# Kernel tuning notes

Measured on AMD Instinct MI355X. Metric: run time of the kernel, lower is better.

## Reference

```python
import jax, jax.numpy as jnp
import numpy as np

DIM = 1024
HEADS = 16
HEAD_DIM = DIM // HEADS
SEQ = 2048
BATCH = 2


def setup_inputs() -> dict:
    key = jax.random.key(0)
    ks = jax.random.split(key, 9)
    s = 1.0 / np.sqrt(DIM)
    mk = lambda k: jax.random.uniform(k, (DIM, DIM), jnp.float32, -s, s)
    mb = lambda k: jax.random.uniform(k, (DIM,), jnp.float32, -s, s)
    return {
        "x": jax.random.normal(ks[0], (BATCH, SEQ, DIM), jnp.float32),
        "wq": mk(ks[1]), "bq": mb(ks[2]),
        "wk": mk(ks[3]), "bk": mb(ks[4]),
        "wv": mk(ks[5]), "bv": mb(ks[6]),
        "wo": mk(ks[7]), "bo": mb(ks[8]),
    }


def reference(x, wq, bq, wk, bk, wv, bv, wo, bo):
    b, s, d = x.shape
    inv_sqrt_hd = 1.0 / np.sqrt(HEAD_DIM)
    # torch Linear: y = x @ W.T + b
    q = (x @ wq.T + bq).reshape(b, s, HEADS, HEAD_DIM)
    k = (x @ wk.T + bk).reshape(b, s, HEADS, HEAD_DIM)
    v = (x @ wv.T + bv).reshape(b, s, HEADS, HEAD_DIM)
    # scores [b, h, s, s]; NOTE: original forward never applies the causal mask buffer
    scores = jnp.einsum("bqhd,bkhd->bhqk", q, k) * inv_sqrt_hd
    a = jax.nn.softmax(scores, axis=-1)
    o = jnp.einsum("bhqk,bkhd->bqhd", a, v).reshape(b, s, d)
    o = o @ wo.T + bo
    return (o, a.mean(axis=1))
```

## Files before the change

kernel.cpp:

```cpp
#include <hip/hip_runtime.h>
#include <stdint.h>

#define DIMD 1024
#define HEADS 16
#define HD 64
#define SEQ 2048
#define BATCH 2
#define MTOT (BATCH*SEQ)

typedef __attribute__((ext_vector_type(4))) float f32x4;
typedef __attribute__((ext_vector_type(8))) short bf16x8;
typedef __attribute__((ext_vector_type(8))) unsigned short ushort8;
typedef __attribute__((ext_vector_type(4))) unsigned short usx4;

#define GL_LDS16(gp, lp) __builtin_amdgcn_global_load_lds( \
    (const __attribute__((address_space(1))) unsigned int*)(gp), \
    (__attribute__((address_space(3))) unsigned int*)(lp), 16, 0, 0)

__device__ __forceinline__ unsigned short f2bf(float f) {
    unsigned int u = __builtin_bit_cast(unsigned int, f);
    u = (u + 0x7FFFu + ((u >> 16) & 1u)) >> 16;
    return (unsigned short)u;
}
__device__ __forceinline__ float bf2f(unsigned short s) {
    unsigned int u = ((unsigned int)s) << 16;
    return __builtin_bit_cast(float, u);
}

__global__ __launch_bounds__(256) void cvt_f32_bf16(const float* __restrict__ in,
                                                    unsigned short* __restrict__ out, int n) {
    int i = (blockIdx.x * 256 + threadIdx.x) * 8;
    if (i >= n) return;
    f32x4 a = *(const f32x4*)(in + i);
    f32x4 b = *(const f32x4*)(in + i + 4);
    ushort8 o;
    o[0] = f2bf(a[0]); o[1] = f2bf(a[1]); o[2] = f2bf(a[2]); o[3] = f2bf(a[3]);
    o[4] = f2bf(b[0]); o[5] = f2bf(b[1]); o[6] = f2bf(b[2]); o[7] = f2bf(b[3]);
    *(ushort8*)(out + i) = o;
}

__global__ __launch_bounds__(256) void cvt_w4(const float* __restrict__ w0, const float* __restrict__ w1,
                                              const float* __restrict__ w2, const float* __restrict__ w3,
                                              unsigned short* __restrict__ dst) {
    const int sel = blockIdx.x >> 9;
    const float* src = sel == 0 ? w0 : sel == 1 ? w1 : sel == 2 ? w2 : w3;
    int i = ((blockIdx.x & 511) * 256 + threadIdx.x) * 8;
    f32x4 a = *(const f32x4*)(src + i);
    f32x4 b = *(const f32x4*)(src + i + 4);
    ushort8 o;
    o[0] = f2bf(a[0]); o[1] = f2bf(a[1]); o[2] = f2bf(a[2]); o[3] = f2bf(a[3]);
    o[4] = f2bf(b[0]); o[5] = f2bf(b[1]); o[6] = f2bf(b[2]); o[7] = f2bf(b[3]);
    *(ushort8*)(dst + (size_t)sel * 1048576 + i) = o;
}

template<bool F32OUT>
__device__ __forceinline__ void gemm_body(const unsigned short* __restrict__ X,
                                          const unsigned short* __restrict__ W,
                                          const float* __restrict__ bias,
                                          void* __restrict__ outp,
                                          int m0, int n0, int Nv, int Kv,
                                          unsigned short (*As)[128 * 64],
                                          unsigned short (*Bs)[64 * 64]) {
    const int tid = threadIdx.x, wid = tid >> 6;
    const int lane = tid & 63, lr = lane & 15, hi = lane >> 4;
    const int mq = (wid >> 1) * 64, nq = (wid & 1) * 32;
    const int NT = Kv >> 6;

    f32x4 acc[4][2];
    #pragma unroll
    for (int i = 0; i < 4; ++i)
        #pragma unroll
        for (int j = 0; j < 2; ++j) acc[i][j] = (f32x4){0.f, 0.f, 0.f, 0.f};

    #pragma unroll
    for (int it = 0; it < 4; ++it) {
        int li = it * 256 + tid, row = li >> 3, seg = li & 7;
        GL_LDS16(X + (size_t)(m0 + row) * Kv + ((seg ^ (row & 7)) << 3), &As[0][li * 8]);
    }
    #pragma unroll
    for (int it = 0; it < 2; ++it) {
        int li = it * 256 + tid, row = li >> 3, seg = li & 7;
        GL_LDS16(W + (size_t)(n0 + row) * Kv + ((seg ^ (row & 7)) << 3), &Bs[0][li * 8]);
    }
    __syncthreads();

    #pragma unroll 2
    for (int t = 0; t < NT; ++t) {
        const int cur = t & 1, nxt = cur ^ 1;
        if (t + 1 < NT) {
            const int k1 = (t + 1) << 6;
            #pragma unroll
            for (int it = 0; it < 4; ++it) {
                int li = it * 256 + tid, row = li >> 3, seg = li & 7;
                GL_LDS16(X + (size_t)(m0 + row) * Kv + k1 + ((seg ^ (row & 7)) << 3),
                         &As[nxt][li * 8]);
            }
            #pragma unroll
            for (int it = 0; it < 2; ++it) {
                int li = it * 256 + tid, row = li >> 3, seg = li & 7;
                GL_LDS16(W + (size_t)(n0 + row) * Kv + k1 + ((seg ^ (row & 7)) << 3),
                         &Bs[nxt][li * 8]);
            }
        }
        #pragma unroll
        for (int kk = 0; kk < 2; ++kk) {
            bf16x8 af[4], bfr[2];
            #pragma unroll
            for (int i = 0; i < 4; ++i) {
                int row = mq + 16 * i + lr;
                int seg = (kk * 4 + hi) ^ (row & 7);
                af[i] = *(const bf16x8*)(&As[cur][row * 64 + seg * 8]);
            }
            #pragma unroll
            for (int j = 0; j < 2; ++j) {
                int row = nq + 16 * j + lr;
                int seg = (kk * 4 + hi) ^ (row & 7);
                bfr[j] = *(const bf16x8*)(&Bs[cur][row * 64 + seg * 8]);
            }
            #pragma unroll
            for (int i = 0; i < 4; ++i)
                #pragma unroll
                for (int j = 0; j < 2; ++j)
                    acc[i][j] = __builtin_amdgcn_mfma_f32_16x16x32_bf16(af[i], bfr[j], acc[i][j], 0, 0, 0);
        }
        __syncthreads();
    }

    #pragma unroll
    for (int j = 0; j < 2; ++j) {
        const int col = n0 + nq + 16 * j + lr;
        const float bv = bias[col];
        #pragma unroll
        for (int i = 0; i < 4; ++i) {
            #pragma unroll
            for (int r = 0; r < 4; ++r) {
                const int row = m0 + mq + 16 * i + 4 * hi + r;
                float v = acc[i][j][r] + bv;
                if (F32OUT) ((float*)outp)[(size_t)row * Nv + col] = v;
                else        ((unsigned short*)outp)[(size_t)row * Nv + col] = f2bf(v);
            }
        }
    }
}

template<bool F32OUT>
__global__ __launch_bounds__(256, 2) void gemm_lds(const unsigned short* __restrict__ X,
                                                   const unsigned short* __restrict__ W,
                                                   const float* __restrict__ bias,
                                                   void* __restrict__ outp,
                                                   int Nv, int Kv) {
    __shared__ unsigned short As[2][128 * 64];
    __shared__ unsigned short Bs[2][64 * 64];
    gemm_body<F32OUT>(X, W, bias, outp, blockIdx.y * 128, blockIdx.x * 64, Nv, Kv, As, Bs);
}

__global__ __launch_bounds__(256, 2) void gemm_qkv(const unsigned short* __restrict__ X,
                                                   const unsigned short* __restrict__ Wall,
                                                   const float* __restrict__ b0,
                                                   const float* __restrict__ b1,
                                                   const float* __restrict__ b2,
                                                   unsigned short* __restrict__ o0,
                                                   unsigned short* __restrict__ o1,
                                                   unsigned short* __restrict__ o2) {
    __shared__ unsigned short As[2][128 * 64];
    __shared__ unsigned short Bs[2][64 * 64];
    const int sel = blockIdx.x >> 4;
    const int n0 = (blockIdx.x & 15) * 64;
    const unsigned short* W = Wall + (size_t)sel * 1048576;
    const float* bias = sel == 0 ? b0 : sel == 1 ? b1 : b2;
    unsigned short* out = sel == 0 ? o0 : sel == 1 ? o1 : o2;
    gemm_body<false>(X, W, bias, out, blockIdx.y * 128, n0, DIMD, DIMD, As, Bs);
}

__global__ __launch_bounds__(256) void transpose_v(const unsigned short* __restrict__ v,
                                                   unsigned short* __restrict__ vT) {
    __shared__ unsigned short tile[64][72];
    const int bh = blockIdx.y;
    const int b = bh >> 4, h = bh & 15;
    const int s0 = blockIdx.x * 64;
    const int t = threadIdx.x;
    #pragma unroll
    for (int it = 0; it < 2; ++it) {
        int li = it * 256 + t;
        int row = li >> 3, c8 = (li & 7) * 8;
        ushort8 val = *(const ushort8*)(v + (size_t)(b * SEQ + s0 + row) * DIMD + h * HD + c8);
        *(ushort8*)&tile[row][c8] = val;
    }
    __syncthreads();
    #pragma unroll
    for (int it = 0; it < 2; ++it) {
        int li = it * 256 + t;
        int d = li >> 3, s8 = (li & 7) * 8;
        ushort8 o;
        #pragma unroll
        for (int j = 0; j < 8; ++j) o[j] = tile[s8 + j][d];
        *(ushort8*)(vT + (size_t)(bh * HD + d) * SEQ + s0 + s8) = o;
    }
}

__global__ __launch_bounds__(256, 4) void score_pv_kernel(const unsigned short* __restrict__ Q,
                                                          const unsigned short* __restrict__ Kt,
                                                          const unsigned short* __restrict__ vT,
                                                          float* __restrict__ rlb,
                                                          unsigned short* __restrict__ attn, int b) {
    __shared__ unsigned short Ks[2][64 * 64];
    __shared__ unsigned short Vs[2][64 * 64];
    __shared__ unsigned short Es[32 * 68];
    __shared__ float ps[4][2][16];
    __shared__ float rls[32];
    const int tid = threadIdx.x, wid = tid >> 6, lane = tid & 63;
    const int lr = lane & 15, hi = lane >> 4;
    const int h = blockIdx.y;
    const int q0 = blockIdx.x * 32;
    const unsigned short* Kbase = Kt + (size_t)b * SEQ * DIMD + h * HD;
    const unsigned short* Vbase = vT + (size_t)(b * HEADS + h) * HD * SEQ;

    const unsigned short* qbase = Q + (size_t)(b * SEQ + q0) * DIMD + h * HD + 8 * hi;
    bf16x8 qb0[2], qb1[2];
    #pragma unroll
    for (int s = 0; s < 2; ++s) {
        const unsigned short* qp = qbase + (size_t)(16 * s + lr) * DIMD;
        qb0[s] = *(const bf16x8*)qp;
        qb1[s] = *(const bf16x8*)(qp + 32);
    }

    #pragma unroll
    for (int it = 0; it < 2; ++it) {
        int li = it * 256 + tid, row = li >> 3, seg = li & 7;
        GL_LDS16(Kbase + (size_t)row * DIMD + ((seg ^ (row & 7)) << 3), &Ks[0][li * 8]);
    }
    #pragma unroll
    for (int it = 0; it < 2; ++it) {
        int li = it * 256 + tid, row = li >> 3, seg = li & 7;
        GL_LDS16(Vbase + (size_t)row * SEQ + ((seg ^ (row & 7)) << 3), &Vs[0][li * 8]);
    }
    __syncthreads();

    float lsum[2] = {0.f, 0.f};
    f32x4 oacc[2];
    oacc[0] = (f32x4){0.f, 0.f, 0.f, 0.f};
    oacc[1] = (f32x4){0.f, 0.f, 0.f, 0.f};
    const int mq = (wid >> 1) * 16;
    const int nd = (wid & 1) * 32;

    for (int t = 0; t < 32; ++t) {
        const int cur = t & 1, nxt = cur ^ 1;
        if (t + 1 < 32) {
            const int kb1 = (t + 1) * 64;
            #pragma unroll
            for (int it = 0; it < 2; ++it) {
                int li = it * 256 + tid, row = li >> 3, seg = li & 7;
                GL_LDS16(Kbase + (size_t)(kb1 + row) * DIMD + ((seg ^ (row & 7)) << 3),
                         &Ks[nxt][li * 8]);
            }
            #pragma unroll
            for (int it = 0; it < 2; ++it) {
                int li = it * 256 + tid, row = li >> 3, seg = li & 7;
                GL_LDS16(Vbase + (size_t)row * SEQ + kb1 + ((seg ^ (row & 7)) << 3),
                         &Vs[nxt][li * 8]);
            }
        }
        const int krow = wid * 16 + lr;
        bf16x8 a0 = *(const bf16x8*)(&Ks[cur][krow * 64 + ((hi       ^ (krow & 7)) << 3)]);
        bf16x8 a1 = *(const bf16x8*)(&Ks[cur][krow * 64 + (((4 + hi) ^ (krow & 7)) << 3)]);
        #pragma unroll
        for (int s = 0; s < 2; ++s) {
            f32x4 acc = (f32x4){0.f, 0.f, 0.f, 0.f};
            acc = __builtin_amdgcn_mfma_f32_16x16x32_bf16(a0, qb0[s], acc, 0, 0, 0);
            acc = __builtin_amdgcn_mfma_f32_16x16x32_bf16(a1, qb1[s], acc, 0, 0, 0);
            float e0 = __expf(acc[0] * 0.125f);
            float e1 = __expf(acc[1] * 0.125f);
            float e2 = __expf(acc[2] * 0.125f);
            float e3 = __expf(acc[3] * 0.125f);
            lsum[s] += (e0 + e1) + (e2 + e3);
            usx4 pk;
            pk[0] = f2bf(e0); pk[1] = f2bf(e1); pk[2] = f2bf(e2); pk[3] = f2bf(e3);
            *(usx4*)(&Es[(16 * s + lr) * 68 + wid * 16 + 4 * hi]) = pk;
        }
        __syncthreads();

        #pragma unroll
        for (int kk = 0; kk < 2; ++kk) {
            bf16x8 ea = *(const bf16x8*)(&Es[(mq + lr) * 68 + kk * 32 + 8 * hi]);
            #pragma unroll
            for (int j = 0; j < 2; ++j) {
                int vrow = nd + 16 * j + lr;
                int seg = (kk * 4 + hi) ^ (vrow & 7);
                bf16x8 vb = *(const bf16x8*)(&Vs[cur][vrow * 64 + seg * 8]);
                oacc[j] = __builtin_amdgcn_mfma_f32_16x16x32_bf16(ea, vb, oacc[j], 0, 0, 0);
            }
        }
        __syncthreads();
    }

    #pragma unroll
    for (int s = 0; s < 2; ++s) {
        float l = lsum[s];
        l += __shfl_xor(l, 16);
        l += __shfl_xor(l, 32);
        if (lane < 16) ps[wid][s][lane] = l;
    }
    __syncthreads();
    if (tid < 32) {
        int s = tid >> 4, qq = tid & 15;
        float tot = ps[0][s][qq] + ps[1][s][qq] + ps[2][s][qq] + ps[3][s][qq];
        float r = 1.0f / tot;
        rlb[h * SEQ + q0 + 16 * s + qq] = r;
        rls[16 * s + qq] = r;
    }
    __syncthreads();

    #pragma unroll
    for (int r = 0; r < 4; ++r) {
        const int ql = mq + 4 * hi + r;
        const float rv = rls[ql];
        #pragma unroll
        for (int j = 0; j < 2; ++j)
            attn[(size_t)(b * SEQ + q0 + ql) * DIMD + h * HD + nd + 16 * j + lr] =
                f2bf(oacc[j][r] * rv);
    }
}

__global__ __launch_bounds__(256, 4) void mean_qk_kernel(const unsigned short* __restrict__ Q,
                                                         const unsigned short* __restrict__ Kt,
                                                         const float* __restrict__ rlb,
                                                         float* __restrict__ out1b, int b) {
    __shared__ unsigned short Ks[2][128 * 64];
    __shared__ unsigned short Qs[2][32 * 64];
    const int tid = threadIdx.x, wid = tid >> 6, lane = tid & 63;
    const int lr = lane & 15, hi = lane >> 4;
    const int k0 = blockIdx.x * 128;
    const int q0 = blockIdx.y * 32;
    const unsigned short* Kb2 = Kt + (size_t)b * SEQ * DIMD;
    const unsigned short* Qb2 = Q + (size_t)(b * SEQ + q0) * DIMD;

    f32x4 acc[2][2];
    #pragma unroll
    for (int c = 0; c < 2; ++c)
        #pragma unroll
        for (int g = 0; g < 2; ++g) acc[c][g] = (f32x4){0.f, 0.f, 0.f, 0.f};

    #pragma unroll
    for (int it = 0; it < 4; ++it) {
        int li = it * 256 + tid, row = li >> 3, seg = li & 7;
        GL_LDS16(Kb2 + (size_t)(k0 + row) * DIMD + ((seg ^ (row & 7)) << 3), &Ks[0][li * 8]);
    }
    {
        int row = tid >> 3, seg = tid & 7;
        GL_LDS16(Qb2 + (size_t)row * DIMD + ((seg ^ (row & 7)) << 3), &Qs[0][tid * 8]);
    }
    __syncthreads();

    for (int h = 0; h < HEADS; ++h) {
        const int cur = h & 1;
        if (h + 1 < HEADS) {
            const int off2 = (h + 1) * HD;
            #pragma unroll
            for (int it = 0; it < 4; ++it) {
                int li = it * 256 + tid, row = li >> 3, seg = li & 7;
                GL_LDS16(Kb2 + (size_t)(k0 + row) * DIMD + off2 + ((seg ^ (row & 7)) << 3),
                         &Ks[cur ^ 1][li * 8]);
            }
            {
                int row = tid >> 3, seg = tid & 7;
                GL_LDS16(Qb2 + (size_t)row * DIMD + off2 + ((seg ^ (row & 7)) << 3),
                         &Qs[cur ^ 1][tid * 8]);
            }
        }
        bf16x8 qb0[2], qb1[2];
        float rlv[2];
        #pragma unroll
        for (int g = 0; g < 2; ++g) {
            const int qrow = 16 * g + lr;
            qb0[g] = *(const bf16x8*)(&Qs[cur][qrow * 64 + ((hi       ^ (qrow & 7)) << 3)]);
            qb1[g] = *(const bf16x8*)(&Qs[cur][qrow * 64 + (((4 + hi) ^ (qrow & 7)) << 3)]);
            rlv[g] = rlb[h * SEQ + q0 + 16 * g + lr] * 0.0625f;
        }
        #pragma unroll
        for (int c = 0; c < 2; ++c) {
            const int krow = c * 64 + wid * 16 + lr;
            bf16x8 a0 = *(const bf16x8*)(&Ks[cur][krow * 64 + ((hi       ^ (krow & 7)) << 3)]);
            bf16x8 a1 = *(const bf16x8*)(&Ks[cur][krow * 64 + (((4 + hi) ^ (krow & 7)) << 3)]);
            #pragma unroll
            for (int g = 0; g < 2; ++g) {
                f32x4 s = (f32x4){0.f, 0.f, 0.f, 0.f};
                s = __builtin_amdgcn_mfma_f32_16x16x32_bf16(a0, qb0[g], s, 0, 0, 0);
                s = __builtin_amdgcn_mfma_f32_16x16x32_bf16(a1, qb1[g], s, 0, 0, 0);
                #pragma unroll
                for (int r = 0; r < 4; ++r)
                    acc[c][g][r] += __expf(s[r] * 0.125f) * rlv[g];
            }
        }
        __syncthreads();
    }

    #pragma unroll
    for (int c = 0; c < 2; ++c)
        #pragma unroll
        for (int g = 0; g < 2; ++g)
            *(f32x4*)(out1b + (size_t)(q0 + 16 * g + lr) * SEQ
                              + k0 + 64 * c + 16 * wid + 4 * hi) = acc[c][g];
}

extern "C" void kernel_launch(void* const* d_in, const int* in_sizes, int n_in,
                              void* d_out, int out_size, void* d_ws, size_t ws_size,
                              hipStream_t stream) {
    const float* x  = (const float*)d_in[0];
    const float* wq = (const float*)d_in[1];
    const float* bq = (const float*)d_in[2];
    const float* wk = (const float*)d_in[3];
    const float* bk = (const float*)d_in[4];
    const float* wv = (const float*)d_in[5];
    const float* bv = (const float*)d_in[6];
    const float* wo = (const float*)d_in[7];
    const float* bo = (const float*)d_in[8];

    float* o_out    = (float*)d_out;
    float* mean_out = o_out + 4194304;

    unsigned short* xb   = (unsigned short*)d_ws;
    unsigned short* wqb  = xb   + 4194304;
    unsigned short* wkb  = wqb  + 1048576;
    unsigned short* wvb  = wkb  + 1048576;
    unsigned short* wob  = wvb  + 1048576;
    unsigned short* qb   = wob  + 1048576;
    unsigned short* kb   = qb   + 4194304;
    unsigned short* vTb  = kb   + 4194304;
    unsigned short* attb = vTb  + 4194304;
    float*          rlb  = (float*)(attb + 4194304);
    unsigned short* vb   = (unsigned short*)(rlb + 65536);

    cvt_f32_bf16<<<2048, 256, 0, stream>>>(x, xb, 4194304);
    cvt_w4<<<2048, 256, 0, stream>>>(wq, wk, wv, wo, wqb);

    gemm_qkv<<<dim3(48, 32), 256, 0, stream>>>(xb, wqb, bq, bk, bv, qb, kb, vb);
    transpose_v<<<dim3(32, 32), 256, 0, stream>>>(vb, vTb);

    for (int b = 0; b < BATCH; ++b) {
        float* rl_b = rlb + b * HEADS * SEQ;
        score_pv_kernel<<<dim3(64, 16), 256, 0, stream>>>(qb, kb, vTb, rl_b, attb, b);
        mean_qk_kernel<<<dim3(16, 64), 256, 0, stream>>>(qb, kb, rl_b,
                                                         mean_out + (size_t)b * SEQ * SEQ, b);
    }

    gemm_lds<true><<<dim3(16, 32), 256, 0, stream>>>(attb, wob, bo, o_out, DIMD, DIMD);
}
```

Measured before the change: 195.2 us.

## Give each wave its own 16 queries in score_pv and merge batch launches

The attention kernel now assigns each wave a private 16-query slice of a 64-query tile. Each wave computes scores over all 64 keys, keeps its own P tile in LDS, and accumulates all 64 output dims, which removes the mid-iteration block barrier and the cross-wave row-sum reduction. The per-batch launch loop is replaced by a 3D grid so both batches run in a single launch of each kernel, which cuts launch count and tail effects. In exchange, per-thread accumulators grow and launch bounds drop to 3 blocks per CU, which lowers occupancy.

After: 202.7 us. +3.9%, slower.

```diff
diff --git a/kernel.cpp b/kernel.cpp
--- a/kernel.cpp
+++ b/kernel.cpp
@@ -198,31 +198,25 @@
     }
 }
 
-__global__ __launch_bounds__(256, 4) void score_pv_kernel(const unsigned short* __restrict__ Q,
+__global__ __launch_bounds__(256, 3) void score_pv_kernel(const unsigned short* __restrict__ Q,
                                                           const unsigned short* __restrict__ Kt,
                                                           const unsigned short* __restrict__ vT,
                                                           float* __restrict__ rlb,
-                                                          unsigned short* __restrict__ attn, int b) {
+                                                          unsigned short* __restrict__ attn) {
     __shared__ unsigned short Ks[2][64 * 64];
     __shared__ unsigned short Vs[2][64 * 64];
-    __shared__ unsigned short Es[32 * 68];
-    __shared__ float ps[4][2][16];
-    __shared__ float rls[32];
+    __shared__ unsigned short Es[4][16 * 68];
     const int tid = threadIdx.x, wid = tid >> 6, lane = tid & 63;
     const int lr = lane & 15, hi = lane >> 4;
     const int h = blockIdx.y;
-    const int q0 = blockIdx.x * 32;
+    const int b = blockIdx.z;
+    const int q0 = blockIdx.x * 64;
     const unsigned short* Kbase = Kt + (size_t)b * SEQ * DIMD + h * HD;
     const unsigned short* Vbase = vT + (size_t)(b * HEADS + h) * HD * SEQ;
 
-    const unsigned short* qbase = Q + (size_t)(b * SEQ + q0) * DIMD + h * HD + 8 * hi;
-    bf16x8 qb0[2], qb1[2];
-    #pragma unroll
-    for (int s = 0; s < 2; ++s) {
-        const unsigned short* qp = qbase + (size_t)(16 * s + lr) * DIMD;
-        qb0[s] = *(const bf16x8*)qp;
-        qb1[s] = *(const bf16x8*)(qp + 32);
-    }
+    const unsigned short* qp = Q + (size_t)(b * SEQ + q0 + 16 * wid + lr) * DIMD + h * HD + 8 * hi;
+    bf16x8 qb0 = *(const bf16x8*)qp;
+    bf16x8 qb1 = *(const bf16x8*)(qp + 32);
 
     #pragma unroll
     for (int it = 0; it < 2; ++it) {
@@ -236,12 +230,11 @@
     }
     __syncthreads();
 
-    float lsum[2] = {0.f, 0.f};
-    f32x4 oacc[2];
-    oacc[0] = (f32x4){0.f, 0.f, 0.f, 0.f};
-    oacc[1] = (f32x4){0.f, 0.f, 0.f, 0.f};
-    const int mq = (wid >> 1) * 16;
-    const int nd = (wid & 1) * 32;
+    float lsum = 0.f;
+    f32x4 oacc[4];
+    #pragma unroll
+    for (int j = 0; j < 4; ++j) oacc[j] = (f32x4){0.f, 0.f, 0.f, 0.f};
+    unsigned short* ew = &Es[wid][0];
 
     for (int t = 0; t < 32; ++t) {
         const int cur = t & 1, nxt = cur ^ 1;
@@ -260,31 +253,29 @@
                          &Vs[nxt][li * 8]);
             }
         }
-        const int krow = wid * 16 + lr;
-        bf16x8 a0 = *(const bf16x8*)(&Ks[cur][krow * 64 + ((hi       ^ (krow & 7)) << 3)]);
-        bf16x8 a1 = *(const bf16x8*)(&Ks[cur][krow * 64 + (((4 + hi) ^ (krow & 7)) << 3)]);
-        #pragma unroll
-        for (int s = 0; s < 2; ++s) {
+        #pragma unroll
+        for (int c = 0; c < 4; ++c) {
+            const int krow = c * 16 + lr;
+            bf16x8 a0 = *(const bf16x8*)(&Ks[cur][krow * 64 + ((hi       ^ (krow & 7)) << 3)]);
+            bf16x8 a1 = *(const bf16x8*)(&Ks[cur][krow * 64 + (((4 + hi) ^ (krow & 7)) << 3)]);
             f32x4 acc = (f32x4){0.f, 0.f, 0.f, 0.f};
-            acc = __builtin_amdgcn_mfma_f32_16x16x32_bf16(a0, qb0[s], acc, 0, 0, 0);
-            acc = __builtin_amdgcn_mfma_f32_16x16x32_bf16(a1, qb1[s], acc, 0, 0, 0);
+            acc = __builtin_amdgcn_mfma_f32_16x16x32_bf16(a0, qb0, acc, 0, 0, 0);
+            acc = __builtin_amdgcn_mfma_f32_16x16x32_bf16(a1, qb1, acc, 0, 0, 0);
             float e0 = __expf(acc[0] * 0.125f);
             float e1 = __expf(acc[1] * 0.125f);
             float e2 = __expf(acc[2] * 0.125f);
             float e3 = __expf(acc[3] * 0.125f);
-            lsum[s] += (e0 + e1) + (e2 + e3);
+            lsum += (e0 + e1) + (e2 + e3);
             usx4 pk;
             pk[0] = f2bf(e0); pk[1] = f2bf(e1); pk[2] = f2bf(e2); pk[3] = f2bf(e3);
-            *(usx4*)(&Es[(16 * s + lr) * 68 + wid * 16 + 4 * hi]) = pk;
-        }
-        __syncthreads();
-
+            *(usx4*)(ew + lr * 68 + c * 16 + 4 * hi) = pk;
+        }
         #pragma unroll
         for (int kk = 0; kk < 2; ++kk) {
-            bf16x8 ea = *(const bf16x8*)(&Es[(mq + lr) * 68 + kk * 32 + 8 * hi]);
-            #pragma unroll
-            for (int j = 0; j < 2; ++j) {
-                int vrow = nd + 16 * j + lr;
+            bf16x8 ea = *(const bf16x8*)(ew + lr * 68 + kk * 32 + 8 * hi);
+            #pragma unroll
+            for (int j = 0; j < 4; ++j) {
+                int vrow = 16 * j + lr;
                 int seg = (kk * 4 + hi) ^ (vrow & 7);
                 bf16x8 vb = *(const bf16x8*)(&Vs[cur][vrow * 64 + seg * 8]);
                 oacc[j] = __builtin_amdgcn_mfma_f32_16x16x32_bf16(ea, vb, oacc[j], 0, 0, 0);
@@ -293,46 +284,39 @@
         __syncthreads();
     }
 
-    #pragma unroll
-    for (int s = 0; s < 2; ++s) {
-        float l = lsum[s];
-        l += __shfl_xor(l, 16);
-        l += __shfl_xor(l, 32);
-        if (lane < 16) ps[wid][s][lane] = l;
-    }
-    __syncthreads();
-    if (tid < 32) {
-        int s = tid >> 4, qq = tid & 15;
-        float tot = ps[0][s][qq] + ps[1][s][qq] + ps[2][s][qq] + ps[3][s][qq];
-        float r = 1.0f / tot;
-        rlb[h * SEQ + q0 + 16 * s + qq] = r;
-        rls[16 * s + qq] = r;
-    }
-    __syncthreads();
+    float l = lsum;
+    l += __shfl_xor(l, 16);
+    l += __shfl_xor(l, 32);
+    float inv = 1.0f / l;
+    if (lane < 16)
+        rlb[(size_t)b * HEADS * SEQ + h * SEQ + q0 + 16 * wid + lane] = inv;
 
     #pragma unroll
     for (int r = 0; r < 4; ++r) {
-        const int ql = mq + 4 * hi + r;
-        const float rv = rls[ql];
-        #pragma unroll
-        for (int j = 0; j < 2; ++j)
-            attn[(size_t)(b * SEQ + q0 + ql) * DIMD + h * HD + nd + 16 * j + lr] =
+        const float rv = __shfl(inv, 4 * hi + r);
+        const int qg = q0 + 16 * wid + 4 * hi + r;
+        #pragma unroll
+        for (int j = 0; j < 4; ++j)
+            attn[(size_t)(b * SEQ + qg) * DIMD + h * HD + 16 * j + lr] =
                 f2bf(oacc[j][r] * rv);
     }
 }
 
 __global__ __launch_bounds__(256, 4) void mean_qk_kernel(const unsigned short* __restrict__ Q,
                                                          const unsigned short* __restrict__ Kt,
-                                                         const float* __restrict__ rlb,
-                                                         float* __restrict__ out1b, int b) {
+                                                         const float* __restrict__ rlb_all,
+                                                         float* __restrict__ out1_all) {
     __shared__ unsigned short Ks[2][128 * 64];
     __shared__ unsigned short Qs[2][32 * 64];
     const int tid = threadIdx.x, wid = tid >> 6, lane = tid & 63;
     const int lr = lane & 15, hi = lane >> 4;
+    const int b = blockIdx.z;
     const int k0 = blockIdx.x * 128;
     const int q0 = blockIdx.y * 32;
     const unsigned short* Kb2 = Kt + (size_t)b * SEQ * DIMD;
     const unsigned short* Qb2 = Q + (size_t)(b * SEQ + q0) * DIMD;
+    const float* rlb = rlb_all + (size_t)b * HEADS * SEQ;
+    float* out1b = out1_all + (size_t)b * SEQ * SEQ;
 
     f32x4 acc[2][2];
     #pragma unroll
@@ -436,12 +420,8 @@
     gemm_qkv<<<dim3(48, 32), 256, 0, stream>>>(xb, wqb, bq, bk, bv, qb, kb, vb);
     transpose_v<<<dim3(32, 32), 256, 0, stream>>>(vb, vTb);
 
-    for (int b = 0; b < BATCH; ++b) {
-        float* rl_b = rlb + b * HEADS * SEQ;
-        score_pv_kernel<<<dim3(64, 16), 256, 0, stream>>>(qb, kb, vTb, rl_b, attb, b);
-        mean_qk_kernel<<<dim3(16, 64), 256, 0, stream>>>(qb, kb, rl_b,
-                                                         mean_out + (size_t)b * SEQ * SEQ, b);
-    }
+    score_pv_kernel<<<dim3(32, 16, 2), 256, 0, stream>>>(qb, kb, vTb, rlb, attb);
+    mean_qk_kernel<<<dim3(16, 64, 2), 256, 0, stream>>>(qb, kb, rlb, mean_out);
 
     gemm_lds<true><<<dim3(16, 32), 256, 0, stream>>>(attb, wob, bo, o_out, DIMD, DIMD);
 }
```
